# Performance work log

Hardware: AMD Instinct MI355X
Metric: run time of the kernel (lower is better)

Reference implementation:

```python
import jax, jax.numpy as jnp
import numpy as np

NUM_HEADS = 16
LN_EPS = 1e-5


def _layer_norm(x, w, b):
    mean = jnp.mean(x, axis=-1, keepdims=True)
    xc = x - mean
    var = jnp.mean(xc * xc, axis=-1, keepdims=True)
    return xc * jax.lax.rsqrt(var + LN_EPS) * w + b


def _triton_softmax(a):
    # Faithful to TritonSoftmax: clamp to [-100,100], stable softmax with
    # +1e-6 in the denominator, then +1e-8 and renormalize.
    a = jnp.clip(a, -100.0, 100.0)
    a = a - jnp.max(a, axis=-1, keepdims=True)
    e = jnp.exp(a)
    p = e / (jnp.sum(e, axis=-1, keepdims=True) + 1e-6)
    p = p + 1e-8
    return p / jnp.sum(p, axis=-1, keepdims=True)


def _triton_gelu(x):
    # y = 0.5*x*(1 + u/(1+|u|)) with u = x * sqrt(2/pi)*(1+0.044715*x^2)
    coeff = 0.7978845608028654 * (1.0 + 0.044715 * x * x)
    u = x * coeff
    return 0.5 * x * (1.0 + u / (1.0 + jnp.abs(u)))


def setup_inputs() -> dict:
    key = jax.random.key(0)
    ks = jax.random.split(key, 6)
    B, T, D = 2, 2048, 1024
    s = 0.02
    return {
        "x": jax.random.normal(ks[0], (B, T, D), jnp.float32),
        "ln1_w": jnp.ones((D,), jnp.float32),
        "ln1_b": jnp.zeros((D,), jnp.float32),
        "ln2_w": jnp.ones((D,), jnp.float32),
        "ln2_b": jnp.zeros((D,), jnp.float32),
        "w_qkv": jax.random.normal(ks[1], (D, 3 * D), jnp.float32) * s,
        "w_proj": jax.random.normal(ks[2], (D, D), jnp.float32) * s,
        "w_ff1": jax.random.normal(ks[3], (D, 4 * D), jnp.float32) * s,
        "w_ff2": jax.random.normal(ks[4], (4 * D, D), jnp.float32) * s,
    }


def reference(x, ln1_w, ln1_b, ln2_w, ln2_b, w_qkv, w_proj, w_ff1, w_ff2):
    B, T, D = x.shape
    H = NUM_HEADS
    hd = D // H
    scale = hd ** -0.5

    # ---- attention sublayer (pre-LN) ----
    h = _layer_norm(x, ln1_w, ln1_b)
    qkv = (h @ w_qkv).reshape(B, T, 3, H, hd).transpose(2, 0, 3, 1, 4)
    q, k, v = qkv[0], qkv[1], qkv[2]  # [B,H,T,hd]
    attn = jnp.einsum("bhqd,bhkd->bhqk", q, k) * scale  # [B,H,T,T]
    causal = jnp.tril(jnp.ones((T, T), bool))
    attn = jnp.where(causal, attn, -jnp.inf)
    attn = _triton_softmax(attn)  # dropout is identity at eval
    o = jnp.einsum("bhqk,bhkd->bhqd", attn, v)
    o = o.transpose(0, 2, 1, 3).reshape(B, T, D)
    x = x + o @ w_proj

    # ---- MLP sublayer (pre-LN) ----
    h = _layer_norm(x, ln2_w, ln2_b)
    x = x + _triton_gelu(h @ w_ff1) @ w_ff2
    return x
```

## Files before the change

kernel.cpp:

```cpp
#include <hip/hip_runtime.h>

typedef __attribute__((ext_vector_type(8))) __bf16 bf16x8;
typedef __attribute__((ext_vector_type(8))) unsigned short u16x8;
typedef __attribute__((ext_vector_type(4))) unsigned short u16x4;
typedef __attribute__((ext_vector_type(4))) float f32x4;

__device__ __forceinline__ unsigned short f2bf(float f) {
  union { float f; unsigned int u; } v; v.f = f;
  unsigned int r = v.u + 0x7fffu + ((v.u >> 16) & 1u);
  return (unsigned short)(r >> 16);
}

__device__ __forceinline__ bf16x8 ldb8(const unsigned short* p) {
  u16x8 u = *(const u16x8*)p;
  return __builtin_bit_cast(bf16x8, u);
}

__device__ __forceinline__ f32x4 mfma16(bf16x8 a, bf16x8 b, f32x4 c) {
  return __builtin_amdgcn_mfma_f32_16x16x32_bf16(a, b, c, 0, 0, 0);
}

__device__ __forceinline__ void gload16(const void* g, void* l) {
  __builtin_amdgcn_global_load_lds(
      (const __attribute__((address_space(1))) void*)g,
      (__attribute__((address_space(3))) void*)l, 16, 0, 0);
}

__device__ __forceinline__ float gelu_t(float x) {
  float u = x * (0.7978845608028654f * (1.0f + 0.044715f * x * x));
  return 0.5f * x * (1.0f + u / (1.0f + fabsf(u)));
}

__global__ __launch_bounds__(256) void tconv_kernel(const float* __restrict__ in,
                                                    unsigned short* __restrict__ out,
                                                    int R, int C) {
  __shared__ unsigned short tile[64][68];
  int r0 = blockIdx.y * 64, c0 = blockIdx.x * 64;
  int tx = threadIdx.x & 63, tg = threadIdx.x >> 6;
  for (int rr = tg; rr < 64; rr += 4)
    tile[tx][rr] = f2bf(in[(size_t)(r0 + rr) * C + c0 + tx]);
  __syncthreads();
  for (int cc = tg; cc < 64; cc += 4)
    out[(size_t)(c0 + cc) * R + r0 + tx] = tile[cc][tx];
}

__global__ __launch_bounds__(256) void vtrans_kernel(const unsigned short* __restrict__ V,
                                                     unsigned short* __restrict__ VT) {
  __shared__ unsigned short tile[64][68];
  int bh = blockIdx.y;
  int t0 = blockIdx.x * 64;
  const unsigned short* in = V + (size_t)bh * 2048 * 64;
  unsigned short* out = VT + (size_t)bh * 64 * 2048;
  int tx = threadIdx.x & 63, tg = threadIdx.x >> 6;
  for (int rr = tg; rr < 64; rr += 4)
    tile[tx][rr] = in[(size_t)(t0 + rr) * 64 + tx];
  __syncthreads();
  for (int dd = tg; dd < 64; dd += 4)
    out[(size_t)dd * 2048 + t0 + tx] = tile[dd][tx];
}

__global__ __launch_bounds__(256) void ln_kernel(const float* __restrict__ X,
                                                 const float* __restrict__ W,
                                                 const float* __restrict__ Bv,
                                                 unsigned short* __restrict__ H) {
  int row = blockIdx.x;
  int t = threadIdx.x;
  float4 v = ((const float4*)(X + (size_t)row * 1024))[t];
  float s = v.x + v.y + v.z + v.w;
  float s2 = v.x * v.x + v.y * v.y + v.z * v.z + v.w * v.w;
#pragma unroll
  for (int m = 32; m >= 1; m >>= 1) { s += __shfl_xor(s, m); s2 += __shfl_xor(s2, m); }
  __shared__ float red[8];
  if ((t & 63) == 0) { red[t >> 6] = s; red[4 + (t >> 6)] = s2; }
  __syncthreads();
  s = red[0] + red[1] + red[2] + red[3];
  s2 = red[4] + red[5] + red[6] + red[7];
  float mean = s * (1.f / 1024.f);
  float var = fmaxf(s2 * (1.f / 1024.f) - mean * mean, 0.f);
  float rs = rsqrtf(var + 1e-5f);
  float4 w4 = ((const float4*)W)[t];
  float4 b4 = ((const float4*)Bv)[t];
  u16x4 o;
  o[0] = f2bf((v.x - mean) * rs * w4.x + b4.x);
  o[1] = f2bf((v.y - mean) * rs * w4.y + b4.y);
  o[2] = f2bf((v.z - mean) * rs * w4.z + b4.z);
  o[3] = f2bf((v.w - mean) * rs * w4.w + b4.w);
  *(u16x4*)(H + (size_t)row * 1024 + t * 4) = o;
}

template <int MODE>
__global__ __launch_bounds__(256) void gemm_kernel(
    const unsigned short* __restrict__ A, const unsigned short* __restrict__ B,
    const float* __restrict__ RES, void* __restrict__ OUT,
    unsigned short* __restrict__ Qo, unsigned short* __restrict__ Ko,
    unsigned short* __restrict__ Vo, int M, int N, int K) {
  __shared__ __align__(16) unsigned short As[128 * 64];
  __shared__ __align__(16) unsigned short Bs[128 * 64];
  const int tid = threadIdx.x;
  const int lane = tid & 63;
  const int wid = __builtin_amdgcn_readfirstlane(tid >> 6);
  const int lane16 = lane & 15, lgrp = lane >> 4;
  const int l8 = lane >> 3;
  const int lb = (lane & 7) * 16;
  const int m0 = blockIdx.y * 128, n0 = blockIdx.x * 128;
  const int wr = wid >> 1, wc = wid & 1;

  f32x4 acc[4][4] = {};

  const char* Ab = (const char*)A + (size_t)m0 * K * 2;
  const char* Bb = (const char*)B + (size_t)n0 * K * 2;
  const size_t rs = (size_t)K * 2;

  for (int k0 = 0; k0 < K; k0 += 64) {
#pragma unroll
    for (int i = 0; i < 4; ++i) {
      int c = wid * 4 + i;
      gload16(Ab + (size_t)(c * 8 + l8) * rs + k0 * 2 + lb, (char*)As + c * 1024);
      gload16(Bb + (size_t)(c * 8 + l8) * rs + k0 * 2 + lb, (char*)Bs + c * 1024);
    }
    asm volatile("s_waitcnt vmcnt(0)" ::: "memory");
    __syncthreads();
#pragma unroll
    for (int ks = 0; ks < 2; ++ks) {
      bf16x8 af[4], bfr[4];
#pragma unroll
      for (int mf = 0; mf < 4; ++mf)
        af[mf] = ldb8(As + (wr * 64 + mf * 16 + lane16) * 64 + ks * 32 + lgrp * 8);
#pragma unroll
      for (int nf = 0; nf < 4; ++nf)
        bfr[nf] = ldb8(Bs + (wc * 64 + nf * 16 + lane16) * 64 + ks * 32 + lgrp * 8);
#pragma unroll
      for (int mf = 0; mf < 4; ++mf)
#pragma unroll
        for (int nf = 0; nf < 4; ++nf)
          acc[mf][nf] = mfma16(af[mf], bfr[nf], acc[mf][nf]);
    }
    __syncthreads();
  }

#pragma unroll
  for (int mf = 0; mf < 4; ++mf) {
    int row = m0 + wr * 64 + mf * 16 + lgrp * 4;
#pragma unroll
    for (int nf = 0; nf < 4; ++nf) {
      int col = n0 + wc * 64 + nf * 16 + lane16;
      if (MODE == 1) {
        float* o = (float*)OUT;
#pragma unroll
        for (int i = 0; i < 4; ++i) {
          size_t idx = (size_t)(row + i) * N + col;
          o[idx] = acc[mf][nf][i] + RES[idx];
        }
      } else if (MODE == 2) {
        unsigned short* o = (unsigned short*)OUT;
#pragma unroll
        for (int i = 0; i < 4; ++i)
          o[(size_t)(row + i) * N + col] = f2bf(gelu_t(acc[mf][nf][i]));
      } else {
        int bI = row >> 11, tI = row & 2047;
        unsigned short* dst;
        int dd;
        if (col < 1024) {
          dst = Qo + (size_t)(bI * 16 + (col >> 6)) * 2048 * 64;
          dd = col & 63;
        } else if (col < 2048) {
          int cc = col - 1024;
          dst = Ko + (size_t)(bI * 16 + (cc >> 6)) * 2048 * 64;
          dd = cc & 63;
        } else {
          int cc = col - 2048;
          dst = Vo + (size_t)(bI * 16 + (cc >> 6)) * 2048 * 64;
          dd = cc & 63;
        }
#pragma unroll
        for (int i = 0; i < 4; ++i)
          dst[(size_t)(tI + i) * 64 + dd] = f2bf(acc[mf][nf][i]);
      }
    }
  }
}

__global__ __launch_bounds__(256) void attn_kernel(const unsigned short* __restrict__ Q,
                                                   const unsigned short* __restrict__ Kb,
                                                   const unsigned short* __restrict__ VT,
                                                   unsigned short* __restrict__ O) {
  __shared__ __align__(16) unsigned short Ks[64 * 64];
  __shared__ __align__(16) unsigned short Vs[64 * 64];
  __shared__ __align__(16) unsigned short Ps[4][32 * 64];
  const int T = 2048;
  const int q0 = ((int)gridDim.x - 1 - (int)blockIdx.x) * 128;
  const int bh = blockIdx.y;
  const int tid = threadIdx.x, lane = tid & 63;
  const int wid = __builtin_amdgcn_readfirstlane(tid >> 6);
  const int lane16 = lane & 15, lgrp = lane >> 4;
  const int l8 = lane >> 3;
  const int swz = ((lane & 7) ^ (l8 & 7)) << 4;

  const int qbase = q0 + wid * 32;
  bf16x8 qf[2][2];
#pragma unroll
  for (int qc = 0; qc < 2; ++qc) {
    const unsigned short* qp = Q + ((size_t)bh * T + qbase + qc * 16 + lane16) * 64;
    qf[qc][0] = ldb8(qp + lgrp * 8);
    qf[qc][1] = ldb8(qp + 32 + lgrp * 8);
  }

  const char* kg = (const char*)(Kb + (size_t)bh * T * 64);
  const char* vg = (const char*)(VT + (size_t)bh * 64 * T);
  char* PsB = (char*)&Ps[wid][0];

  f32x4 acc_o[2][4] = {};
  float m_run[2] = {-1e30f, -1e30f};
  float l_run[2] = {0.f, 0.f};

  const int nkv = q0 / 64 + 2;
  for (int kt = 0; kt < nkv; ++kt) {
    const int kv0 = kt * 64;
#pragma unroll
    for (int i = 0; i < 2; ++i) {
      int c = wid * 2 + i;
      gload16(kg + (size_t)(kv0 + c * 8 + l8) * 128 + swz, (char*)Ks + c * 1024);
      gload16(vg + (size_t)(c * 8 + l8) * (T * 2) + (size_t)kv0 * 2 + swz, (char*)Vs + c * 1024);
    }
    asm volatile("s_waitcnt vmcnt(0)" ::: "memory");
    __syncthreads();

    bf16x8 kf[4][2], vf[4][2];
#pragma unroll
    for (int f = 0; f < 4; ++f)
#pragma unroll
      for (int c = 0; c < 2; ++c) {
        int row = f * 16 + lane16;
        int off = (c * 64 + lgrp * 16) ^ ((row & 7) << 4);
        kf[f][c] = ldb8((const unsigned short*)((const char*)Ks + row * 128 + off));
        vf[f][c] = ldb8((const unsigned short*)((const char*)Vs + row * 128 + off));
      }

#pragma unroll
    for (int qc = 0; qc < 2; ++qc) {
      const int qrow = qbase + qc * 16 + lane16;
      f32x4 accs[4] = {};
      __builtin_amdgcn_s_setprio(1);
#pragma unroll
      for (int kvf = 0; kvf < 4; ++kvf)
#pragma unroll
        for (int c = 0; c < 2; ++c)
          accs[kvf] = mfma16(kf[kvf][c], qf[qc][c], accs[kvf]);
      __builtin_amdgcn_s_setprio(0);

      float p[16];
      float tmax = -1e30f;
#pragma unroll
      for (int kvf = 0; kvf < 4; ++kvf)
#pragma unroll
        for (int i = 0; i < 4; ++i) {
          int kv = kv0 + kvf * 16 + lgrp * 4 + i;
          float sv = accs[kvf][i] * 0.125f;
          sv = (kv > qrow) ? -1e30f : sv;
          p[kvf * 4 + i] = sv;
          tmax = fmaxf(tmax, sv);
        }
      tmax = fmaxf(tmax, __shfl_xor(tmax, 16));
      tmax = fmaxf(tmax, __shfl_xor(tmax, 32));
      float m_new = fmaxf(m_run[qc], tmax);
      float corr = __expf(m_run[qc] - m_new);
      float psum = 0.f;
#pragma unroll
      for (int j = 0; j < 16; ++j) { p[j] = __expf(p[j] - m_new); psum += p[j]; }
      psum += __shfl_xor(psum, 16);
      psum += __shfl_xor(psum, 32);
      l_run[qc] = l_run[qc] * corr + psum;
      m_run[qc] = m_new;
      float cf0 = __shfl(corr, lgrp * 4 + 0);
      float cf1 = __shfl(corr, lgrp * 4 + 1);
      float cf2 = __shfl(corr, lgrp * 4 + 2);
      float cf3 = __shfl(corr, lgrp * 4 + 3);
#pragma unroll
      for (int df = 0; df < 4; ++df) {
        acc_o[qc][df][0] *= cf0; acc_o[qc][df][1] *= cf1;
        acc_o[qc][df][2] *= cf2; acc_o[qc][df][3] *= cf3;
      }
      const int prow = qc * 16 + lane16;
#pragma unroll
      for (int kvf = 0; kvf < 4; ++kvf) {
        u16x4 pk;
#pragma unroll
        for (int i = 0; i < 4; ++i) pk[i] = f2bf(p[kvf * 4 + i]);
        *(u16x4*)(PsB + prow * 128 + ((kvf * 32 + lgrp * 8) ^ ((prow & 7) << 4))) = pk;
      }
      bf16x8 pf[2];
#pragma unroll
      for (int c = 0; c < 2; ++c)
        pf[c] = ldb8((const unsigned short*)(PsB + prow * 128 +
                     ((c * 64 + lgrp * 16) ^ ((prow & 7) << 4))));
      __builtin_amdgcn_s_setprio(1);
#pragma unroll
      for (int c = 0; c < 2; ++c)
#pragma unroll
        for (int df = 0; df < 4; ++df)
          acc_o[qc][df] = mfma16(pf[c], vf[df][c], acc_o[qc][df]);
      __builtin_amdgcn_s_setprio(0);
    }
    __syncthreads();
  }

  const int b = bh >> 4, hh = bh & 15;
#pragma unroll
  for (int qc = 0; qc < 2; ++qc) {
    float il = 1.f / l_run[qc];
    float f0 = __shfl(il, lgrp * 4 + 0);
    float f1 = __shfl(il, lgrp * 4 + 1);
    float f2 = __shfl(il, lgrp * 4 + 2);
    float f3 = __shfl(il, lgrp * 4 + 3);
#pragma unroll
    for (int df = 0; df < 4; ++df) {
      int col = hh * 64 + df * 16 + lane16;
      size_t base = ((size_t)(b * T + qbase + qc * 16 + lgrp * 4)) * 1024 + col;
      O[base] = f2bf(acc_o[qc][df][0] * f0);
      O[base + 1024] = f2bf(acc_o[qc][df][1] * f1);
      O[base + 2048] = f2bf(acc_o[qc][df][2] * f2);
      O[base + 3072] = f2bf(acc_o[qc][df][3] * f3);
    }
  }
}

extern "C" void kernel_launch(void* const* d_in, const int* in_sizes, int n_in,
                              void* d_out, int out_size, void* d_ws, size_t ws_size,
                              hipStream_t stream) {
  (void)in_sizes; (void)n_in; (void)out_size; (void)ws_size;
  const float* x    = (const float*)d_in[0];
  const float* ln1w = (const float*)d_in[1];
  const float* ln1b = (const float*)d_in[2];
  const float* ln2w = (const float*)d_in[3];
  const float* ln2b = (const float*)d_in[4];
  const float* wqkv = (const float*)d_in[5];
  const float* wprj = (const float*)d_in[6];
  const float* wff1 = (const float*)d_in[7];
  const float* wff2 = (const float*)d_in[8];
  float* out = (float*)d_out;
  char* ws = (char*)d_ws;

  unsigned short* h      = (unsigned short*)(ws + 0);
  unsigned short* wqkvT  = (unsigned short*)(ws + 8388608);
  unsigned short* wprjT  = (unsigned short*)(ws + 14680064);
  unsigned short* wff1T  = (unsigned short*)(ws + 16777216);
  unsigned short* wff2T  = (unsigned short*)(ws + 25165824);
  unsigned short* qb     = (unsigned short*)(ws + 33554432);
  unsigned short* kb     = (unsigned short*)(ws + 41943040);
  unsigned short* vT     = (unsigned short*)(ws + 50331648);
  unsigned short* ob     = (unsigned short*)(ws + 58720256);
  unsigned short* h2     = (unsigned short*)(ws + 67108864);
  unsigned short* a1     = (unsigned short*)(ws + 75497472);
  unsigned short* vo     = h2;

  tconv_kernel<<<dim3(48, 16), 256, 0, stream>>>(wqkv, wqkvT, 1024, 3072);
  tconv_kernel<<<dim3(16, 16), 256, 0, stream>>>(wprj, wprjT, 1024, 1024);
  tconv_kernel<<<dim3(64, 16), 256, 0, stream>>>(wff1, wff1T, 1024, 4096);
  tconv_kernel<<<dim3(16, 64), 256, 0, stream>>>(wff2, wff2T, 4096, 1024);

  ln_kernel<<<4096, 256, 0, stream>>>(x, ln1w, ln1b, h);
  gemm_kernel<0><<<dim3(24, 32), 256, 0, stream>>>(h, wqkvT, nullptr, nullptr,
                                                   qb, kb, vo, 4096, 3072, 1024);
  vtrans_kernel<<<dim3(32, 32), 256, 0, stream>>>(vo, vT);
  attn_kernel<<<dim3(16, 32), 256, 0, stream>>>(qb, kb, vT, ob);
  gemm_kernel<1><<<dim3(8, 32), 256, 0, stream>>>(ob, wprjT, x, out,
                                                  nullptr, nullptr, nullptr, 4096, 1024, 1024);
  ln_kernel<<<4096, 256, 0, stream>>>(out, ln2w, ln2b, h2);
  gemm_kernel<2><<<dim3(32, 32), 256, 0, stream>>>(h2, wff1T, nullptr, a1,
                                                   nullptr, nullptr, nullptr, 4096, 4096, 1024);
  gemm_kernel<1><<<dim3(8, 32), 256, 0, stream>>>(a1, wff2T, out, out,
                                                  nullptr, nullptr, nullptr, 4096, 1024, 4096);
}
```

Baseline: 429.2 us.

## Double-buffer GEMM/attention LDS tiles and streamline online softmax with lazy rescale

The two N=1024 projection GEMMs and the attention kernel now double-buffer their LDS tiles: the next K/V or A/B tile is issued right after the barrier, so global loads overlap with MFMA work, and one barrier per iteration is dropped. In attention, the softmax moves to base-2 exponentials with a folded scale, skips the causal mask on fully unmasked tiles, and rescales the running max only when the new max exceeds the old one by more than a threshold. f2bf now uses the hardware bf16 conversion. The costs are doubled LDS use, which may lower occupancy, and the lazy-rescale threshold, which lets exponentials grow up to 2^8 before renormalisation.

```diff
diff --git a/kernel.cpp b/kernel.cpp
--- a/kernel.cpp
+++ b/kernel.cpp
@@ -6,9 +6,7 @@
 typedef __attribute__((ext_vector_type(4))) float f32x4;
 
 __device__ __forceinline__ unsigned short f2bf(float f) {
-  union { float f; unsigned int u; } v; v.f = f;
-  unsigned int r = v.u + 0x7fffu + ((v.u >> 16) & 1u);
-  return (unsigned short)(r >> 16);
+  return __builtin_bit_cast(unsigned short, (__bf16)f);
 }
 
 __device__ __forceinline__ bf16x8 ldb8(const unsigned short* p) {
@@ -88,14 +86,14 @@
   *(u16x4*)(H + (size_t)row * 1024 + t * 4) = o;
 }
 
-template <int MODE>
+template <int MODE, bool DBUF>
 __global__ __launch_bounds__(256) void gemm_kernel(
     const unsigned short* __restrict__ A, const unsigned short* __restrict__ B,
     const float* __restrict__ RES, void* __restrict__ OUT,
     unsigned short* __restrict__ Qo, unsigned short* __restrict__ Ko,
     unsigned short* __restrict__ Vo, int M, int N, int K) {
-  __shared__ __align__(16) unsigned short As[128 * 64];
-  __shared__ __align__(16) unsigned short Bs[128 * 64];
+  __shared__ __align__(16) unsigned short As[DBUF ? 2 : 1][128 * 64];
+  __shared__ __align__(16) unsigned short Bs[DBUF ? 2 : 1][128 * 64];
   const int tid = threadIdx.x;
   const int lane = tid & 63;
   const int wid = __builtin_amdgcn_readfirstlane(tid >> 6);
@@ -111,31 +109,49 @@
   const char* Bb = (const char*)B + (size_t)n0 * K * 2;
   const size_t rs = (size_t)K * 2;
 
-  for (int k0 = 0; k0 < K; k0 += 64) {
+  auto stage = [&](int k0, int b) {
 #pragma unroll
     for (int i = 0; i < 4; ++i) {
       int c = wid * 4 + i;
-      gload16(Ab + (size_t)(c * 8 + l8) * rs + k0 * 2 + lb, (char*)As + c * 1024);
-      gload16(Bb + (size_t)(c * 8 + l8) * rs + k0 * 2 + lb, (char*)Bs + c * 1024);
-    }
-    asm volatile("s_waitcnt vmcnt(0)" ::: "memory");
-    __syncthreads();
+      gload16(Ab + (size_t)(c * 8 + l8) * rs + (size_t)k0 * 2 + lb,
+              (char*)&As[0][0] + b * 16384 + c * 1024);
+      gload16(Bb + (size_t)(c * 8 + l8) * rs + (size_t)k0 * 2 + lb,
+              (char*)&Bs[0][0] + b * 16384 + c * 1024);
+    }
+  };
+
+  const int kIt = K / 64;
+  if (DBUF) stage(0, 0);
+
+  for (int it = 0; it < kIt; ++it) {
+    int cur;
+    if (DBUF) {
+      cur = it & 1;
+      asm volatile("s_waitcnt vmcnt(0)" ::: "memory");
+      __syncthreads();
+      if (it + 1 < kIt) stage((it + 1) * 64, cur ^ 1);
+    } else {
+      cur = 0;
+      stage(it * 64, 0);
+      asm volatile("s_waitcnt vmcnt(0)" ::: "memory");
+      __syncthreads();
+    }
 #pragma unroll
     for (int ks = 0; ks < 2; ++ks) {
       bf16x8 af[4], bfr[4];
 #pragma unroll
       for (int mf = 0; mf < 4; ++mf)
-        af[mf] = ldb8(As + (wr * 64 + mf * 16 + lane16) * 64 + ks * 32 + lgrp * 8);
+        af[mf] = ldb8(&As[cur][(wr * 64 + mf * 16 + lane16) * 64 + ks * 32 + lgrp * 8]);
 #pragma unroll
       for (int nf = 0; nf < 4; ++nf)
-        bfr[nf] = ldb8(Bs + (wc * 64 + nf * 16 + lane16) * 64 + ks * 32 + lgrp * 8);
+        bfr[nf] = ldb8(&Bs[cur][(wc * 64 + nf * 16 + lane16) * 64 + ks * 32 + lgrp * 8]);
 #pragma unroll
       for (int mf = 0; mf < 4; ++mf)
 #pragma unroll
         for (int nf = 0; nf < 4; ++nf)
           acc[mf][nf] = mfma16(af[mf], bfr[nf], acc[mf][nf]);
     }
-    __syncthreads();
+    if (!DBUF) __syncthreads();
   }
 
 #pragma unroll
@@ -184,8 +200,8 @@
                                                    const unsigned short* __restrict__ Kb,
                                                    const unsigned short* __restrict__ VT,
                                                    unsigned short* __restrict__ O) {
-  __shared__ __align__(16) unsigned short Ks[64 * 64];
-  __shared__ __align__(16) unsigned short Vs[64 * 64];
+  __shared__ __align__(16) unsigned short Ks[2][64 * 64];
+  __shared__ __align__(16) unsigned short Vs[2][64 * 64];
   __shared__ __align__(16) unsigned short Ps[4][32 * 64];
   const int T = 2048;
   const int q0 = ((int)gridDim.x - 1 - (int)blockIdx.x) * 128;
@@ -195,6 +211,7 @@
   const int lane16 = lane & 15, lgrp = lane >> 4;
   const int l8 = lane >> 3;
   const int swz = ((lane & 7) ^ (l8 & 7)) << 4;
+  const float SCL2 = 0.18033688011112042f;
 
   const int qbase = q0 + wid * 32;
   bf16x8 qf[2][2];
@@ -209,21 +226,32 @@
   const char* vg = (const char*)(VT + (size_t)bh * 64 * T);
   char* PsB = (char*)&Ps[wid][0];
 
+  auto stage = [&](int kv0, int b) {
+#pragma unroll
+    for (int i = 0; i < 2; ++i) {
+      int c = wid * 2 + i;
+      gload16(kg + (size_t)(kv0 + c * 8 + l8) * 128 + swz,
+              (char*)&Ks[0][0] + b * 8192 + c * 1024);
+      gload16(vg + (size_t)(c * 8 + l8) * (T * 2) + (size_t)kv0 * 2 + swz,
+              (char*)&Vs[0][0] + b * 8192 + c * 1024);
+    }
+  };
+
   f32x4 acc_o[2][4] = {};
   float m_run[2] = {-1e30f, -1e30f};
   float l_run[2] = {0.f, 0.f};
 
   const int nkv = q0 / 64 + 2;
+  stage(0, 0);
   for (int kt = 0; kt < nkv; ++kt) {
     const int kv0 = kt * 64;
-#pragma unroll
-    for (int i = 0; i < 2; ++i) {
-      int c = wid * 2 + i;
-      gload16(kg + (size_t)(kv0 + c * 8 + l8) * 128 + swz, (char*)Ks + c * 1024);
-      gload16(vg + (size_t)(c * 8 + l8) * (T * 2) + (size_t)kv0 * 2 + swz, (char*)Vs + c * 1024);
-    }
+    const int cur = kt & 1;
     asm volatile("s_waitcnt vmcnt(0)" ::: "memory");
     __syncthreads();
+    if (kt + 1 < nkv) stage((kt + 1) * 64, cur ^ 1);
+
+    const char* KsB = (const char*)&Ks[0][0] + cur * 8192;
+    const char* VsB = (const char*)&Vs[0][0] + cur * 8192;
 
     bf16x8 kf[4][2], vf[4][2];
 #pragma unroll
@@ -232,8 +260,8 @@
       for (int c = 0; c < 2; ++c) {
         int row = f * 16 + lane16;
         int off = (c * 64 + lgrp * 16) ^ ((row & 7) << 4);
-        kf[f][c] = ldb8((const unsigned short*)((const char*)Ks + row * 128 + off));
-        vf[f][c] = ldb8((const unsigned short*)((const char*)Vs + row * 128 + off));
+        kf[f][c] = ldb8((const unsigned short*)(KsB + row * 128 + off));
+        vf[f][c] = ldb8((const unsigned short*)(VsB + row * 128 + off));
       }
 
 #pragma unroll
@@ -248,38 +276,53 @@
           accs[kvf] = mfma16(kf[kvf][c], qf[qc][c], accs[kvf]);
       __builtin_amdgcn_s_setprio(0);
 
-      float p[16];
-      float tmax = -1e30f;
-#pragma unroll
-      for (int kvf = 0; kvf < 4; ++kvf)
-#pragma unroll
-        for (int i = 0; i < 4; ++i) {
-          int kv = kv0 + kvf * 16 + lgrp * 4 + i;
-          float sv = accs[kvf][i] * 0.125f;
-          sv = (kv > qrow) ? -1e30f : sv;
-          p[kvf * 4 + i] = sv;
-          tmax = fmaxf(tmax, sv);
-        }
+      float sc[16];
+      if (kv0 + 64 <= qbase + qc * 16) {
+#pragma unroll
+        for (int kvf = 0; kvf < 4; ++kvf)
+#pragma unroll
+          for (int i = 0; i < 4; ++i)
+            sc[kvf * 4 + i] = accs[kvf][i] * SCL2;
+      } else {
+#pragma unroll
+        for (int kvf = 0; kvf < 4; ++kvf)
+#pragma unroll
+          for (int i = 0; i < 4; ++i) {
+            int kv = kv0 + kvf * 16 + lgrp * 4 + i;
+            float v = accs[kvf][i] * SCL2;
+            sc[kvf * 4 + i] = (kv > qrow) ? -1e30f : v;
+          }
+      }
+      float tmax = sc[0];
+#pragma unroll
+      for (int j = 1; j < 16; ++j) tmax = fmaxf(tmax, sc[j]);
       tmax = fmaxf(tmax, __shfl_xor(tmax, 16));
       tmax = fmaxf(tmax, __shfl_xor(tmax, 32));
-      float m_new = fmaxf(m_run[qc], tmax);
-      float corr = __expf(m_run[qc] - m_new);
+      float m_c = m_run[qc];
+      if (!__all(tmax <= m_c + 8.f)) {
+        float m_new = fmaxf(m_c, tmax);
+        float corr = exp2f(m_c - m_new);
+        l_run[qc] *= corr;
+        float cf0 = __shfl(corr, lgrp * 4 + 0);
+        float cf1 = __shfl(corr, lgrp * 4 + 1);
+        float cf2 = __shfl(corr, lgrp * 4 + 2);
+        float cf3 = __shfl(corr, lgrp * 4 + 3);
+#pragma unroll
+        for (int df = 0; df < 4; ++df) {
+          acc_o[qc][df][0] *= cf0; acc_o[qc][df][1] *= cf1;
+          acc_o[qc][df][2] *= cf2; acc_o[qc][df][3] *= cf3;
+        }
+        m_run[qc] = m_new;
+        m_c = m_new;
+      }
+      float p[16];
       float psum = 0.f;
 #pragma unroll
-      for (int j = 0; j < 16; ++j) { p[j] = __expf(p[j] - m_new); psum += p[j]; }
+      for (int j = 0; j < 16; ++j) { p[j] = exp2f(sc[j] - m_c); psum += p[j]; }
       psum += __shfl_xor(psum, 16);
       psum += __shfl_xor(psum, 32);
-      l_run[qc] = l_run[qc] * corr + psum;
-      m_run[qc] = m_new;
-      float cf0 = __shfl(corr, lgrp * 4 + 0);
-      float cf1 = __shfl(corr, lgrp * 4 + 1);
-      float cf2 = __shfl(corr, lgrp * 4 + 2);
-      float cf3 = __shfl(corr, lgrp * 4 + 3);
-#pragma unroll
-      for (int df = 0; df < 4; ++df) {
-        acc_o[qc][df][0] *= cf0; acc_o[qc][df][1] *= cf1;
-        acc_o[qc][df][2] *= cf2; acc_o[qc][df][3] *= cf3;
-      }
+      l_run[qc] += psum;
+
       const int prow = qc * 16 + lane16;
 #pragma unroll
       for (int kvf = 0; kvf < 4; ++kvf) {
@@ -301,7 +344,6 @@
           acc_o[qc][df] = mfma16(pf[c], vf[df][c], acc_o[qc][df]);
       __builtin_amdgcn_s_setprio(0);
     }
-    __syncthreads();
   }
 
   const int b = bh >> 4, hh = bh & 15;
@@ -359,15 +401,15 @@
   tconv_kernel<<<dim3(16, 64), 256, 0, stream>>>(wff2, wff2T, 4096, 1024);
 
   ln_kernel<<<4096, 256, 0, stream>>>(x, ln1w, ln1b, h);
-  gemm_kernel<0><<<dim3(24, 32), 256, 0, stream>>>(h, wqkvT, nullptr, nullptr,
-                                                   qb, kb, vo, 4096, 3072, 1024);
+  gemm_kernel<0, false><<<dim3(24, 32), 256, 0, stream>>>(h, wqkvT, nullptr, nullptr,
+                                                          qb, kb, vo, 4096, 3072, 1024);
   vtrans_kernel<<<dim3(32, 32), 256, 0, stream>>>(vo, vT);
   attn_kernel<<<dim3(16, 32), 256, 0, stream>>>(qb, kb, vT, ob);
-  gemm_kernel<1><<<dim3(8, 32), 256, 0, stream>>>(ob, wprjT, x, out,
-                                                  nullptr, nullptr, nullptr, 4096, 1024, 1024);
+  gemm_kernel<1, true><<<dim3(8, 32), 256, 0, stream>>>(ob, wprjT, x, out,
+                                                        nullptr, nullptr, nullptr, 4096, 1024, 1024);
   ln_kernel<<<4096, 256, 0, stream>>>(out, ln2w, ln2b, h2);
-  gemm_kernel<2><<<dim3(32, 32), 256, 0, stream>>>(h2, wff1T, nullptr, a1,
-                                                   nullptr, nullptr, nullptr, 4096, 4096, 1024);
-  gemm_kernel<1><<<dim3(8, 32), 256, 0, stream>>>(a1, wff2T, out, out,
-                                                  nullptr, nullptr, nullptr, 4096, 1024, 4096);
-}
+  gemm_kernel<2, false><<<dim3(32, 32), 256, 0, stream>>>(h2, wff1T, nullptr, a1,
+                                                          nullptr, nullptr, nullptr, 4096, 4096, 1024);
+  gemm_kernel<1, true><<<dim3(8, 32), 256, 0, stream>>>(a1, wff2T, out, out,
+                                                        nullptr, nullptr, nullptr, 4096, 1024, 4096);
+}
```

Result: no change. 426.1 us (-0.7%).
